# Kernel tuning notes

Hardware: AMD Instinct MI355X
Metric: run time of the kernel (lower is better)

## Reference

```python
import jax, jax.numpy as jnp
import numpy as np

B, T, D = 2, 2048, 1024
N_HEADS = 16
HEAD_DIM = D // N_HEADS


def setup_inputs() -> dict:
    key = jax.random.key(0)
    ks = jax.random.split(key, 5)
    s = 0.02
    return {
        "x": jax.random.normal(ks[0], (B, T, D), jnp.float32),
        "wq": jax.random.normal(ks[1], (D, D), jnp.float32) * s,
        "wk": jax.random.normal(ks[2], (D, D), jnp.float32) * s,
        "wv": jax.random.normal(ks[3], (D, D), jnp.float32) * s,
        "wo": jax.random.normal(ks[4], (D, D), jnp.float32) * s,
        "bo": jnp.zeros((D,), jnp.float32),
    }


def reference(x, wq, wk, wv, wo, bo):
    b, t, _ = x.shape
    # QKV projections (weights stored [d_in, d_out]); reshape to (b, heads, t, head_dim)
    def split_heads(y):
        return y.reshape(b, t, N_HEADS, HEAD_DIM).transpose(0, 2, 1, 3)
    q = split_heads(x @ wq)
    k = split_heads(x @ wk)
    v = split_heads(x @ wv)
    # causal attention scores: (b, h, t, t)
    scores = jnp.einsum("bhqd,bhkd->bhqk", q, k)
    causal = jnp.tril(jnp.ones((t, t), bool))  # True where attending allowed
    scores = jnp.where(causal, scores, -jnp.inf)
    attn = jax.nn.softmax(scores / np.sqrt(HEAD_DIM).astype(np.float32), axis=-1)
    # dropout_rate = 0.0 (eval mode) -> identity
    ctx = jnp.einsum("bhqk,bhkd->bhqd", attn, v)
    ctx = ctx.transpose(0, 2, 1, 3).reshape(b, t, D)
    return ctx @ wo + bo
```

## Files before the change

kernel.cpp:

```cpp
#include <hip/hip_runtime.h>
#include <hip/hip_bf16.h>
#include <cstdint>

typedef __hip_bfloat16 bf16;
typedef __bf16 bf16x8 __attribute__((ext_vector_type(8)));
typedef __bf16 bf16x4 __attribute__((ext_vector_type(4)));
typedef float f32x4 __attribute__((ext_vector_type(4)));
typedef uint32_t u32x4 __attribute__((ext_vector_type(4)));

#define LOG2E 1.4426950408889634f

__device__ __forceinline__ void gload_lds16(const void* g, void* l) {
  __builtin_amdgcn_global_load_lds(
      (const __attribute__((address_space(1))) unsigned int*)g,
      (__attribute__((address_space(3))) unsigned int*)l,
      16, 0, 0);
}

__device__ __forceinline__ uint32_t pack_bf16(float a, float b) {
  const uint32_t ha = (uint32_t)__builtin_bit_cast(uint16_t, (__bf16)a);
  const uint32_t hb = (uint32_t)__builtin_bit_cast(uint16_t, (__bf16)b);
  return ha | (hb << 16);
}

__global__ void conv_k(const float* __restrict__ src, bf16* __restrict__ dst, int n) {
  const int i = (blockIdx.x * 256 + threadIdx.x) * 8;
  if (i >= n) return;
  const f32x4 a = *(const f32x4*)(src + i);
  const f32x4 b = *(const f32x4*)(src + i + 4);
  bf16x8 o;
#pragma unroll
  for (int j = 0; j < 4; ++j) { o[j] = (__bf16)a[j]; o[4 + j] = (__bf16)b[j]; }
  *(bf16x8*)(dst + i) = o;
}

__global__ void transpose_conv4(
    const float* __restrict__ wq, const float* __restrict__ wk,
    const float* __restrict__ wv, const float* __restrict__ wo,
    bf16* __restrict__ dqkv, bf16* __restrict__ dout) {
  __shared__ float tile[32][33];
  const int z = blockIdx.z;
  const float* src = (z == 0) ? wq : ((z == 1) ? wk : ((z == 2) ? wv : wo));
  bf16* dst = (z < 3) ? (dqkv + (long)z * 1048576) : dout;
  const int bx = blockIdx.x * 32, by = blockIdx.y * 32;
  const int tx = threadIdx.x;
  for (int j = threadIdx.y; j < 32; j += 8)
    tile[j][tx] = src[(long)(by + j) * 1024 + bx + tx];
  __syncthreads();
  for (int j = threadIdx.y; j < 32; j += 8)
    dst[(long)(bx + j) * 1024 + by + tx] = __float2bfloat16(tile[tx][j]);
}

__global__ __launch_bounds__(256, 2) void gemm_qkv(
    const bf16* __restrict__ A, const bf16* __restrict__ Bt,
    bf16* __restrict__ Cq, bf16* __restrict__ Ck, bf16* __restrict__ Cv,
    int M, int N, int K) {
  __shared__ __align__(16) bf16 As[128 * 64];
  __shared__ __align__(16) bf16 Bs[128 * 64];

  const int tid = threadIdx.x;
  const int lane = tid & 63;
  const int wave = tid >> 6;
  const int quad = lane >> 4;
  const int l16 = lane & 15;
  const int id = (int)blockIdx.y * 24 + (int)blockIdx.x;
  const int xcd = id & 7, idx = id >> 3;
  const int bxn = xcd * 3 + idx % 3;
  const int byn = idx / 3;
  const int m0 = byn * 128;
  const int n0 = bxn * 128;
  const int wm = (wave >> 1) * 64;
  const int wn = (wave & 1) * 64;

  const f32x4 zero4 = {0.f, 0.f, 0.f, 0.f};
  f32x4 acc[4][4];
#pragma unroll
  for (int mi = 0; mi < 4; ++mi)
#pragma unroll
    for (int ni = 0; ni < 4; ++ni) acc[mi][ni] = zero4;

  const int sRow = tid >> 3;
  const int sK = (tid & 7) * 8;
  const int sSwz = sK ^ (8 * (sRow & 7));
  const bf16* Ag = A + (long)(m0 + sRow) * K + sSwz;
  const bf16* Bg = Bt + (long)(n0 + sRow) * K + sSwz;
  const int swzr = 8 * (l16 & 7);

  for (int k0 = 0; k0 < K; k0 += 64) {
#pragma unroll
    for (int j = 0; j < 4; ++j) {
      gload_lds16(Ag + k0 + (long)(32 * j) * K, &As[tid * 8 + 2048 * j]);
      gload_lds16(Bg + k0 + (long)(32 * j) * K, &Bs[tid * 8 + 2048 * j]);
    }
    __syncthreads();

#pragma unroll
    for (int ks = 0; ks < 64; ks += 32) {
      const int colr = (ks + quad * 8) ^ swzr;
      bf16x8 af[4], bfv[4];
#pragma unroll
      for (int mi = 0; mi < 4; ++mi)
        af[mi] = *(const bf16x8*)&As[(wm + mi * 16 + l16) * 64 + colr];
#pragma unroll
      for (int ni = 0; ni < 4; ++ni)
        bfv[ni] = *(const bf16x8*)&Bs[(wn + ni * 16 + l16) * 64 + colr];
#pragma unroll
      for (int mi = 0; mi < 4; ++mi)
#pragma unroll
        for (int ni = 0; ni < 4; ++ni)
          acc[mi][ni] = __builtin_amdgcn_mfma_f32_16x16x32_bf16(af[mi], bfv[ni], acc[mi][ni], 0, 0, 0);
    }
    __syncthreads();
  }

#pragma unroll
  for (int mi = 0; mi < 4; ++mi) {
    const int gmb = m0 + wm + mi * 16 + quad * 4;
#pragma unroll
    for (int ni = 0; ni < 4; ++ni) {
      const int n = n0 + wn + ni * 16 + l16;
      const int which = n >> 10, rem = n & 1023;
      const int h = rem >> 6, hd = rem & 63;
      bf16* dst = (which == 0) ? Cq : ((which == 1) ? Ck : Cv);
#pragma unroll
      for (int r = 0; r < 4; ++r) {
        const int gm = gmb + r;
        const int b = gm >> 11, t = gm & 2047;
        dst[(((long)(b * 16 + h)) * 2048 + t) * 64 + hd] = __float2bfloat16(acc[mi][ni][r]);
      }
    }
  }
}

__global__ __launch_bounds__(256, 3) void gemm_out(
    const bf16* __restrict__ A, const bf16* __restrict__ Bt,
    const float* __restrict__ bias, float* __restrict__ Cout,
    int M, int N, int K) {
  __shared__ __align__(16) bf16 As[64 * 32];
  __shared__ __align__(16) bf16 Bs[128 * 32];

  const int tid = threadIdx.x;
  const int lane = tid & 63;
  const int wave = tid >> 6;
  const int quad = lane >> 4;
  const int l16 = lane & 15;
  const int id = (int)blockIdx.y * 8 + (int)blockIdx.x;
  const int m0 = (id >> 3) * 64;
  const int n0 = (id & 7) * 128;
  const int wm = (wave & 1) * 32;
  const int wn = (wave >> 1) * 64;

  const f32x4 zero4 = {0.f, 0.f, 0.f, 0.f};
  f32x4 acc[2][4];
#pragma unroll
  for (int mi = 0; mi < 2; ++mi)
#pragma unroll
    for (int ni = 0; ni < 4; ++ni) acc[mi][ni] = zero4;

  const int sRow = tid >> 2;
  const int sK = (tid & 3) * 8;
  const bf16* Ag = A + (long)(m0 + sRow) * K + sK;
  const bf16* Bg = Bt + (long)(n0 + sRow) * K + sK;
  const bf16* Bg2 = Bg + 64L * K;

  for (int k0 = 0; k0 < K; k0 += 32) {
    gload_lds16(Ag + k0, &As[tid * 8]);
    gload_lds16(Bg + k0, &Bs[tid * 8]);
    gload_lds16(Bg2 + k0, &Bs[tid * 8 + 2048]);
    __syncthreads();

    bf16x8 af[2], bfv[4];
#pragma unroll
    for (int mi = 0; mi < 2; ++mi)
      af[mi] = *(const bf16x8*)&As[(wm + mi * 16 + l16) * 32 + quad * 8];
#pragma unroll
    for (int ni = 0; ni < 4; ++ni)
      bfv[ni] = *(const bf16x8*)&Bs[(wn + ni * 16 + l16) * 32 + quad * 8];
#pragma unroll
    for (int mi = 0; mi < 2; ++mi)
#pragma unroll
      for (int ni = 0; ni < 4; ++ni)
        acc[mi][ni] = __builtin_amdgcn_mfma_f32_16x16x32_bf16(af[mi], bfv[ni], acc[mi][ni], 0, 0, 0);
    __syncthreads();
  }

#pragma unroll
  for (int mi = 0; mi < 2; ++mi) {
    const int gmb = m0 + wm + mi * 16 + quad * 4;
#pragma unroll
    for (int ni = 0; ni < 4; ++ni) {
      const int n = n0 + wn + ni * 16 + l16;
      const float bv = bias[n];
#pragma unroll
      for (int r = 0; r < 4; ++r)
        Cout[(long)(gmb + r) * N + n] = acc[mi][ni][r] + bv;
    }
  }
}

__global__ __launch_bounds__(256, 3) void attn_kernel(
    const bf16* __restrict__ Q, const bf16* __restrict__ Kg, const bf16* __restrict__ Vg,
    bf16* __restrict__ ctx) {
  constexpr int KSTR = 72, VSTR = 136;
  __shared__ __align__(16) bf16 Ks[128 * KSTR];
  __shared__ __align__(16) bf16 Vt[64 * VSTR];

  const int tid = threadIdx.x;
  const int lane = tid & 63;
  const int wave = tid >> 6;
  const int quad = lane >> 4;
  const int l16 = lane & 15;

  const int id = (int)blockIdx.y * 16 + (int)blockIdx.x;
  const int g = id & 7;
  const int bh = g * 4 + ((id >> 3) & 3);
  const int p = id >> 5;

  const long base = (long)bh * 2048 * 64;
  const int b = bh >> 4, h = bh & 15;

  const int krow = tid >> 1;
  const int kc32 = (tid & 1) * 32;
  const int vr4 = (tid & 31) * 4;
  const int vd8 = (tid >> 5) * 8;
  const int vb4 = (vr4 >> 4) & 1;
  const int vc4 = (vr4 & ~31) + 8 * (((vr4 >> 2) & 3) ^ vb4) + 4 * vb4;

  const float negsh = -12.0f * LOG2E;
  const f32x4 zero4 = {0.f, 0.f, 0.f, 0.f};

#pragma unroll 1
  for (int seg = 0; seg < 2; ++seg) {
    const int qt = seg ? (31 - p) : p;
    const int qbase = qt * 64 + wave * 16;
    const int q = qbase + l16;

    bf16x8 qf0 = *(const bf16x8*)(Q + base + (long)(qbase + l16) * 64 + quad * 8);
    bf16x8 qf1 = *(const bf16x8*)(Q + base + (long)(qbase + l16) * 64 + 32 + quad * 8);
#pragma unroll
    for (int j = 0; j < 8; ++j) {
      qf0[j] = (__bf16)((float)qf0[j] * 0.125f);
      qf1[j] = (__bf16)((float)qf1[j] * 0.125f);
    }

    float l_i = 0.f;
    f32x4 oacc[4];
#pragma unroll
    for (int nb = 0; nb < 4; ++nb) oacc[nb] = zero4;

    const int nk = (qt + 2) >> 1;
    bf16x8 kr[4], vv[4];
    {
      const bf16* kp = Kg + base + (long)krow * 64 + kc32;
#pragma unroll
      for (int i = 0; i < 4; ++i) kr[i] = *(const bf16x8*)(kp + i * 8);
#pragma unroll
      for (int i = 0; i < 4; ++i)
        vv[i] = *(const bf16x8*)(Vg + base + (long)(vr4 + i) * 64 + vd8);
    }

    for (int kt = 0; kt < nk; ++kt) {
      const int k0 = kt * 128;
#pragma unroll
      for (int i = 0; i < 4; ++i)
        *(bf16x8*)&Ks[krow * KSTR + kc32 + i * 8] = kr[i];
#pragma unroll
      for (int j = 0; j < 8; ++j) {
        bf16x4 t;
        t[0] = vv[0][j]; t[1] = vv[1][j]; t[2] = vv[2][j]; t[3] = vv[3][j];
        *(bf16x4*)&Vt[(vd8 + j) * VSTR + vc4] = t;
      }
      __syncthreads();
      if (kt + 1 < nk) {
        const bf16* kp = Kg + base + (long)(k0 + 128 + krow) * 64 + kc32;
#pragma unroll
        for (int i = 0; i < 4; ++i) kr[i] = *(const bf16x8*)(kp + i * 8);
#pragma unroll
        for (int i = 0; i < 4; ++i)
          vv[i] = *(const bf16x8*)(Vg + base + (long)(k0 + 128 + vr4 + i) * 64 + vd8);
      }

      f32x4 s8[8];
      __builtin_amdgcn_s_setprio(1);
#pragma unroll
      for (int kb = 0; kb < 8; ++kb) {
        const bf16x8 kb0 = *(const bf16x8*)&Ks[(kb * 16 + l16) * KSTR + quad * 8];
        const bf16x8 kb1 = *(const bf16x8*)&Ks[(kb * 16 + l16) * KSTR + 32 + quad * 8];
        f32x4 a = zero4;
        a = __builtin_amdgcn_mfma_f32_16x16x32_bf16(kb0, qf0, a, 0, 0, 0);
        a = __builtin_amdgcn_mfma_f32_16x16x32_bf16(kb1, qf1, a, 0, 0, 0);
        s8[kb] = a;
      }
      __builtin_amdgcn_s_setprio(0);

      if (kt == nk - 1) {
        const int qg = q - k0 - quad * 4;
#pragma unroll
        for (int kb = 0; kb < 8; ++kb)
#pragma unroll
          for (int r = 0; r < 4; ++r)
            s8[kb][r] = (kb * 16 + r <= qg) ? s8[kb][r] : -1e30f;
      }

      float rsum = 0.f;
      u32x4 paw[4];
#pragma unroll
      for (int kk = 0; kk < 4; ++kk) {
        const float p0 = exp2f(fmaf(s8[2 * kk][0], LOG2E, negsh));
        const float p1 = exp2f(fmaf(s8[2 * kk][1], LOG2E, negsh));
        const float p2 = exp2f(fmaf(s8[2 * kk][2], LOG2E, negsh));
        const float p3 = exp2f(fmaf(s8[2 * kk][3], LOG2E, negsh));
        const float p4 = exp2f(fmaf(s8[2 * kk + 1][0], LOG2E, negsh));
        const float p5 = exp2f(fmaf(s8[2 * kk + 1][1], LOG2E, negsh));
        const float p6 = exp2f(fmaf(s8[2 * kk + 1][2], LOG2E, negsh));
        const float p7 = exp2f(fmaf(s8[2 * kk + 1][3], LOG2E, negsh));
        rsum += ((p0 + p1) + (p2 + p3)) + ((p4 + p5) + (p6 + p7));
        u32x4 w;
        w[0] = pack_bf16(p0, p1);
        w[1] = pack_bf16(p2, p3);
        w[2] = (uint32_t)__shfl_xor((int)pack_bf16(p4, p5), 16);
        w[3] = (uint32_t)__shfl_xor((int)pack_bf16(p6, p7), 16);
        paw[kk] = w;
      }

      __builtin_amdgcn_s_setprio(1);
#pragma unroll
      for (int kk = 0; kk < 4; ++kk) {
        const bf16x8 pa = __builtin_bit_cast(bf16x8, paw[kk]);
#pragma unroll
        for (int nb2 = 0; nb2 < 4; ++nb2) {
          const bf16x8 vb = *(const bf16x8*)&Vt[(nb2 * 16 + l16) * VSTR + kk * 32 + quad * 8];
          oacc[nb2] = __builtin_amdgcn_mfma_f32_16x16x32_bf16(pa, vb, oacc[nb2], 0, 0, 0);
        }
      }
      __builtin_amdgcn_s_setprio(0);

      rsum += __shfl_xor(rsum, 16);
      rsum += __shfl_xor(rsum, 32);
      l_i += rsum;
      __syncthreads();
    }

    float linv[4];
#pragma unroll
    for (int r = 0; r < 4; ++r) linv[r] = 1.0f / __shfl(l_i, quad * 4 + r);
#pragma unroll
    for (int r = 0; r < 4; ++r) {
      const int t = qbase + quad * 4 + r;
#pragma unroll
      for (int nb2 = 0; nb2 < 4; ++nb2) {
        const int d = h * 64 + nb2 * 16 + l16;
        ctx[((long)b * 2048 + t) * 1024 + d] = __float2bfloat16(oacc[nb2][r] * linv[r]);
      }
    }
  }
}

extern "C" void kernel_launch(void* const* d_in, const int* in_sizes, int n_in,
                              void* d_out, int out_size, void* d_ws, size_t ws_size,
                              hipStream_t stream) {
  const float* x  = (const float*)d_in[0];
  const float* wq = (const float*)d_in[1];
  const float* wk = (const float*)d_in[2];
  const float* wv = (const float*)d_in[3];
  const float* wo = (const float*)d_in[4];
  const float* bo = (const float*)d_in[5];
  float* out = (float*)d_out;

  bf16* Wtqkv = (bf16*)d_ws;
  bf16* Wto   = Wtqkv + 3145728;
  bf16* xb    = Wto + 1048576;
  bf16* Qb    = xb + 4194304;
  bf16* Kb    = Qb + 4194304;
  bf16* Vb    = Kb + 4194304;
  bf16* Cx    = xb;

  hipLaunchKernelGGL(conv_k, dim3(2048), dim3(256), 0, stream, x, xb, 4194304);
  hipLaunchKernelGGL(transpose_conv4, dim3(32, 32, 4), dim3(32, 8), 0, stream,
                     wq, wk, wv, wo, Wtqkv, Wto);

  hipLaunchKernelGGL(gemm_qkv, dim3(24, 32), dim3(256), 0, stream,
                     xb, Wtqkv, Qb, Kb, Vb, 4096, 3072, 1024);

  hipLaunchKernelGGL(attn_kernel, dim3(16, 32), dim3(256), 0, stream, Qb, Kb, Vb, Cx);

  hipLaunchKernelGGL(gemm_out, dim3(8, 64), dim3(256), 0, stream,
                     Cx, Wto, bo, out, 4096, 1024, 1024);
}
```

Measured before the change: 182.3 us.

## Process two adjacent query tiles per block to share K/V tile loads

Restructures the attention kernel so each block handles one 128-row query tile as two 64-row halves sharing each staged K/V tile. Before, a block ran two separate 64-row tiles (p and 31-p) in sequence and reloaded K/V for each. The change cuts global and LDS traffic per query and interleaves two independent MFMA chains. In exchange, per-block work is now uneven across the causal triangle rather than balanced by pairing, and register pressure is higher, so launch bounds drop from 3 to 2 blocks per CU.

```diff
diff --git a/kernel.cpp b/kernel.cpp
--- a/kernel.cpp
+++ b/kernel.cpp
@@ -21,6 +21,30 @@
   const uint32_t ha = (uint32_t)__builtin_bit_cast(uint16_t, (__bf16)a);
   const uint32_t hb = (uint32_t)__builtin_bit_cast(uint16_t, (__bf16)b);
   return ha | (hb << 16);
+}
+
+__device__ __forceinline__ float softmax_pack(const f32x4 (&s8)[8], u32x4 (&paw)[4],
+                                              float negsh) {
+  float rsum = 0.f;
+#pragma unroll
+  for (int kk = 0; kk < 4; ++kk) {
+    const float p0 = exp2f(fmaf(s8[2 * kk][0], LOG2E, negsh));
+    const float p1 = exp2f(fmaf(s8[2 * kk][1], LOG2E, negsh));
+    const float p2 = exp2f(fmaf(s8[2 * kk][2], LOG2E, negsh));
+    const float p3 = exp2f(fmaf(s8[2 * kk][3], LOG2E, negsh));
+    const float p4 = exp2f(fmaf(s8[2 * kk + 1][0], LOG2E, negsh));
+    const float p5 = exp2f(fmaf(s8[2 * kk + 1][1], LOG2E, negsh));
+    const float p6 = exp2f(fmaf(s8[2 * kk + 1][2], LOG2E, negsh));
+    const float p7 = exp2f(fmaf(s8[2 * kk + 1][3], LOG2E, negsh));
+    rsum += ((p0 + p1) + (p2 + p3)) + ((p4 + p5) + (p6 + p7));
+    u32x4 w;
+    w[0] = pack_bf16(p0, p1);
+    w[1] = pack_bf16(p2, p3);
+    w[2] = (uint32_t)__shfl_xor((int)pack_bf16(p4, p5), 16);
+    w[3] = (uint32_t)__shfl_xor((int)pack_bf16(p6, p7), 16);
+    paw[kk] = w;
+  }
+  return rsum;
 }
 
 __global__ void conv_k(const float* __restrict__ src, bf16* __restrict__ dst, int n) {
@@ -198,7 +222,7 @@
   }
 }
 
-__global__ __launch_bounds__(256, 3) void attn_kernel(
+__global__ __launch_bounds__(256, 2) void attn_kernel(
     const bf16* __restrict__ Q, const bf16* __restrict__ Kg, const bf16* __restrict__ Vg,
     bf16* __restrict__ ctx) {
   constexpr int KSTR = 72, VSTR = 136;
@@ -214,10 +238,32 @@
   const int id = (int)blockIdx.y * 16 + (int)blockIdx.x;
   const int g = id & 7;
   const int bh = g * 4 + ((id >> 3) & 3);
-  const int p = id >> 5;
+  const int pp = id >> 5;
+  const int tq = (pp < 8) ? pp : 23 - pp;
 
   const long base = (long)bh * 2048 * 64;
   const int b = bh >> 4, h = bh & 15;
+
+  const int qbaseA = tq * 128 + wave * 16;
+  const int qbaseB = qbaseA + 64;
+
+  bf16x8 qfA0 = *(const bf16x8*)(Q + base + (long)(qbaseA + l16) * 64 + quad * 8);
+  bf16x8 qfA1 = *(const bf16x8*)(Q + base + (long)(qbaseA + l16) * 64 + 32 + quad * 8);
+  bf16x8 qfB0 = *(const bf16x8*)(Q + base + (long)(qbaseB + l16) * 64 + quad * 8);
+  bf16x8 qfB1 = *(const bf16x8*)(Q + base + (long)(qbaseB + l16) * 64 + 32 + quad * 8);
+#pragma unroll
+  for (int j = 0; j < 8; ++j) {
+    qfA0[j] = (__bf16)((float)qfA0[j] * 0.125f);
+    qfA1[j] = (__bf16)((float)qfA1[j] * 0.125f);
+    qfB0[j] = (__bf16)((float)qfB0[j] * 0.125f);
+    qfB1[j] = (__bf16)((float)qfB1[j] * 0.125f);
+  }
+
+  const f32x4 zero4 = {0.f, 0.f, 0.f, 0.f};
+  float l_iA = 0.f, l_iB = 0.f;
+  f32x4 oaccA[4], oaccB[4];
+#pragma unroll
+  for (int nb = 0; nb < 4; ++nb) { oaccA[nb] = zero4; oaccB[nb] = zero4; }
 
   const int krow = tid >> 1;
   const int kc32 = (tid & 1) * 32;
@@ -227,130 +273,118 @@
   const int vc4 = (vr4 & ~31) + 8 * (((vr4 >> 2) & 3) ^ vb4) + 4 * vb4;
 
   const float negsh = -12.0f * LOG2E;
-  const f32x4 zero4 = {0.f, 0.f, 0.f, 0.f};
-
-#pragma unroll 1
-  for (int seg = 0; seg < 2; ++seg) {
-    const int qt = seg ? (31 - p) : p;
-    const int qbase = qt * 64 + wave * 16;
-    const int q = qbase + l16;
-
-    bf16x8 qf0 = *(const bf16x8*)(Q + base + (long)(qbase + l16) * 64 + quad * 8);
-    bf16x8 qf1 = *(const bf16x8*)(Q + base + (long)(qbase + l16) * 64 + 32 + quad * 8);
+
+  const int nk = tq + 1;
+  bf16x8 kr[4], vv[4];
+  {
+    const bf16* kp = Kg + base + (long)krow * 64 + kc32;
+#pragma unroll
+    for (int i = 0; i < 4; ++i) kr[i] = *(const bf16x8*)(kp + i * 8);
+#pragma unroll
+    for (int i = 0; i < 4; ++i)
+      vv[i] = *(const bf16x8*)(Vg + base + (long)(vr4 + i) * 64 + vd8);
+  }
+
+  for (int kt = 0; kt < nk; ++kt) {
+    const int k0 = kt * 128;
+#pragma unroll
+    for (int i = 0; i < 4; ++i)
+      *(bf16x8*)&Ks[krow * KSTR + kc32 + i * 8] = kr[i];
 #pragma unroll
     for (int j = 0; j < 8; ++j) {
-      qf0[j] = (__bf16)((float)qf0[j] * 0.125f);
-      qf1[j] = (__bf16)((float)qf1[j] * 0.125f);
-    }
-
-    float l_i = 0.f;
-    f32x4 oacc[4];
-#pragma unroll
-    for (int nb = 0; nb < 4; ++nb) oacc[nb] = zero4;
-
-    const int nk = (qt + 2) >> 1;
-    bf16x8 kr[4], vv[4];
-    {
-      const bf16* kp = Kg + base + (long)krow * 64 + kc32;
+      bf16x4 t;
+      t[0] = vv[0][j]; t[1] = vv[1][j]; t[2] = vv[2][j]; t[3] = vv[3][j];
+      *(bf16x4*)&Vt[(vd8 + j) * VSTR + vc4] = t;
+    }
+    __syncthreads();
+    if (kt + 1 < nk) {
+      const bf16* kp = Kg + base + (long)(k0 + 128 + krow) * 64 + kc32;
 #pragma unroll
       for (int i = 0; i < 4; ++i) kr[i] = *(const bf16x8*)(kp + i * 8);
 #pragma unroll
       for (int i = 0; i < 4; ++i)
-        vv[i] = *(const bf16x8*)(Vg + base + (long)(vr4 + i) * 64 + vd8);
-    }
-
-    for (int kt = 0; kt < nk; ++kt) {
-      const int k0 = kt * 128;
-#pragma unroll
-      for (int i = 0; i < 4; ++i)
-        *(bf16x8*)&Ks[krow * KSTR + kc32 + i * 8] = kr[i];
-#pragma unroll
-      for (int j = 0; j < 8; ++j) {
-        bf16x4 t;
-        t[0] = vv[0][j]; t[1] = vv[1][j]; t[2] = vv[2][j]; t[3] = vv[3][j];
-        *(bf16x4*)&Vt[(vd8 + j) * VSTR + vc4] = t;
+        vv[i] = *(const bf16x8*)(Vg + base + (long)(k0 + 128 + vr4 + i) * 64 + vd8);
+    }
+
+    f32x4 sA[8], sB[8];
+    __builtin_amdgcn_s_setprio(1);
+#pragma unroll
+    for (int kb = 0; kb < 8; ++kb) {
+      const bf16x8 kb0 = *(const bf16x8*)&Ks[(kb * 16 + l16) * KSTR + quad * 8];
+      const bf16x8 kb1 = *(const bf16x8*)&Ks[(kb * 16 + l16) * KSTR + 32 + quad * 8];
+      f32x4 aA = zero4, aB = zero4;
+      aA = __builtin_amdgcn_mfma_f32_16x16x32_bf16(kb0, qfA0, aA, 0, 0, 0);
+      aB = __builtin_amdgcn_mfma_f32_16x16x32_bf16(kb0, qfB0, aB, 0, 0, 0);
+      aA = __builtin_amdgcn_mfma_f32_16x16x32_bf16(kb1, qfA1, aA, 0, 0, 0);
+      aB = __builtin_amdgcn_mfma_f32_16x16x32_bf16(kb1, qfB1, aB, 0, 0, 0);
+      sA[kb] = aA; sB[kb] = aB;
+    }
+    __builtin_amdgcn_s_setprio(0);
+
+    if (kt == nk - 1) {
+      const int qgA = wave * 16 + l16 - quad * 4;
+      const int qgB = qgA + 64;
+#pragma unroll
+      for (int kb = 0; kb < 8; ++kb)
+#pragma unroll
+        for (int r = 0; r < 4; ++r) {
+          sA[kb][r] = (kb * 16 + r <= qgA) ? sA[kb][r] : -1e30f;
+          sB[kb][r] = (kb * 16 + r <= qgB) ? sB[kb][r] : -1e30f;
+        }
+    }
+
+    u32x4 pawA[4], pawB[4];
+    float rsumA = softmax_pack(sA, pawA, negsh);
+    float rsumB = softmax_pack(sB, pawB, negsh);
+
+    __builtin_amdgcn_s_setprio(1);
+#pragma unroll
+    for (int kk = 0; kk < 4; ++kk) {
+      const bf16x8 paA = __builtin_bit_cast(bf16x8, pawA[kk]);
+      const bf16x8 paB = __builtin_bit_cast(bf16x8, pawB[kk]);
+#pragma unroll
+      for (int nb2 = 0; nb2 < 4; ++nb2) {
+        const bf16x8 vb = *(const bf16x8*)&Vt[(nb2 * 16 + l16) * VSTR + kk * 32 + quad * 8];
+        oaccA[nb2] = __builtin_amdgcn_mfma_f32_16x16x32_bf16(paA, vb, oaccA[nb2], 0, 0, 0);
+        oaccB[nb2] = __builtin_amdgcn_mfma_f32_16x16x32_bf16(paB, vb, oaccB[nb2], 0, 0, 0);
       }
-      __syncthreads();
-      if (kt + 1 < nk) {
-        const bf16* kp = Kg + base + (long)(k0 + 128 + krow) * 64 + kc32;
-#pragma unroll
-        for (int i = 0; i < 4; ++i) kr[i] = *(const bf16x8*)(kp + i * 8);
-#pragma unroll
-        for (int i = 0; i < 4; ++i)
-          vv[i] = *(const bf16x8*)(Vg + base + (long)(k0 + 128 + vr4 + i) * 64 + vd8);
-      }
-
-      f32x4 s8[8];
-      __builtin_amdgcn_s_setprio(1);
-#pragma unroll
-      for (int kb = 0; kb < 8; ++kb) {
-        const bf16x8 kb0 = *(const bf16x8*)&Ks[(kb * 16 + l16) * KSTR + quad * 8];
-        const bf16x8 kb1 = *(const bf16x8*)&Ks[(kb * 16 + l16) * KSTR + 32 + quad * 8];
-        f32x4 a = zero4;
-        a = __builtin_amdgcn_mfma_f32_16x16x32_bf16(kb0, qf0, a, 0, 0, 0);
-        a = __builtin_amdgcn_mfma_f32_16x16x32_bf16(kb1, qf1, a, 0, 0, 0);
-        s8[kb] = a;
-      }
-      __builtin_amdgcn_s_setprio(0);
-
-      if (kt == nk - 1) {
-        const int qg = q - k0 - quad * 4;
-#pragma unroll
-        for (int kb = 0; kb < 8; ++kb)
-#pragma unroll
-          for (int r = 0; r < 4; ++r)
-            s8[kb][r] = (kb * 16 + r <= qg) ? s8[kb][r] : -1e30f;
-      }
-
-      float rsum = 0.f;
-      u32x4 paw[4];
-#pragma unroll
-      for (int kk = 0; kk < 4; ++kk) {
-        const float p0 = exp2f(fmaf(s8[2 * kk][0], LOG2E, negsh));
-        const float p1 = exp2f(fmaf(s8[2 * kk][1], LOG2E, negsh));
-        const float p2 = exp2f(fmaf(s8[2 * kk][2], LOG2E, negsh));
-        const float p3 = exp2f(fmaf(s8[2 * kk][3], LOG2E, negsh));
-        const float p4 = exp2f(fmaf(s8[2 * kk + 1][0], LOG2E, negsh));
-        const float p5 = exp2f(fmaf(s8[2 * kk + 1][1], LOG2E, negsh));
-        const float p6 = exp2f(fmaf(s8[2 * kk + 1][2], LOG2E, negsh));
-        const float p7 = exp2f(fmaf(s8[2 * kk + 1][3], LOG2E, negsh));
-        rsum += ((p0 + p1) + (p2 + p3)) + ((p4 + p5) + (p6 + p7));
-        u32x4 w;
-        w[0] = pack_bf16(p0, p1);
-        w[1] = pack_bf16(p2, p3);
-        w[2] = (uint32_t)__shfl_xor((int)pack_bf16(p4, p5), 16);
-        w[3] = (uint32_t)__shfl_xor((int)pack_bf16(p6, p7), 16);
-        paw[kk] = w;
-      }
-
-      __builtin_amdgcn_s_setprio(1);
-#pragma unroll
-      for (int kk = 0; kk < 4; ++kk) {
-        const bf16x8 pa = __builtin_bit_cast(bf16x8, paw[kk]);
-#pragma unroll
-        for (int nb2 = 0; nb2 < 4; ++nb2) {
-          const bf16x8 vb = *(const bf16x8*)&Vt[(nb2 * 16 + l16) * VSTR + kk * 32 + quad * 8];
-          oacc[nb2] = __builtin_amdgcn_mfma_f32_16x16x32_bf16(pa, vb, oacc[nb2], 0, 0, 0);
-        }
-      }
-      __builtin_amdgcn_s_setprio(0);
-
-      rsum += __shfl_xor(rsum, 16);
-      rsum += __shfl_xor(rsum, 32);
-      l_i += rsum;
-      __syncthreads();
-    }
-
+    }
+    __builtin_amdgcn_s_setprio(0);
+
+    rsumA += __shfl_xor(rsumA, 16);
+    rsumA += __shfl_xor(rsumA, 32);
+    l_iA += rsumA;
+    rsumB += __shfl_xor(rsumB, 16);
+    rsumB += __shfl_xor(rsumB, 32);
+    l_iB += rsumB;
+    __syncthreads();
+  }
+
+  {
     float linv[4];
 #pragma unroll
-    for (int r = 0; r < 4; ++r) linv[r] = 1.0f / __shfl(l_i, quad * 4 + r);
+    for (int r = 0; r < 4; ++r) linv[r] = 1.0f / __shfl(l_iA, quad * 4 + r);
 #pragma unroll
     for (int r = 0; r < 4; ++r) {
-      const int t = qbase + quad * 4 + r;
+      const int t = qbaseA + quad * 4 + r;
 #pragma unroll
       for (int nb2 = 0; nb2 < 4; ++nb2) {
         const int d = h * 64 + nb2 * 16 + l16;
-        ctx[((long)b * 2048 + t) * 1024 + d] = __float2bfloat16(oacc[nb2][r] * linv[r]);
+        ctx[((long)b * 2048 + t) * 1024 + d] = __float2bfloat16(oaccA[nb2][r] * linv[r]);
+      }
+    }
+  }
+  {
+    float linv[4];
+#pragma unroll
+    for (int r = 0; r < 4; ++r) linv[r] = 1.0f / __shfl(l_iB, quad * 4 + r);
+#pragma unroll
+    for (int r = 0; r < 4; ++r) {
+      const int t = qbaseB + quad * 4 + r;
+#pragma unroll
+      for (int nb2 = 0; nb2 < 4; ++nb2) {
+        const int d = h * 64 + nb2 * 16 + l16;
+        ctx[((long)b * 2048 + t) * 1024 + d] = __float2bfloat16(oaccB[nb2][r] * linv[r]);
       }
     }
   }
```

After: 188.5 us. 3.4% more time.
